# Kernel optimization log

Hardware: AMD Instinct MI355X
Metric: run time of the kernel (lower is better)

## Reference

```python
import jax, jax.numpy as jnp
import numpy as np

N_NODES = 50000
N_EDGES = 800000
D_IN = 64
D_OUT = 64


def setup_inputs() -> dict:
    key = jax.random.key(0)
    ks = jax.random.split(key, 5)
    feat = jax.random.normal(ks[0], (N_NODES, D_IN), dtype=jnp.float32)
    src = jax.random.randint(ks[1], (N_EDGES,), 0, N_NODES, dtype=jnp.int64)
    dst = jax.random.randint(ks[2], (N_EDGES,), 0, N_NODES, dtype=jnp.int64)
    # Xavier-uniform-ish scale for weights
    lim = float(np.sqrt(6.0 / (D_IN + D_OUT)) * np.sqrt(2.0))
    W_neigh = jax.random.uniform(ks[3], (D_OUT, D_IN), dtype=jnp.float32, minval=-lim, maxval=lim)
    W_self = jax.random.uniform(ks[4], (D_OUT, D_IN), dtype=jnp.float32, minval=-lim, maxval=lim)
    b_self = jnp.zeros((D_OUT,), dtype=jnp.float32)
    return {"feat": feat, "src": src, "dst": dst,
            "W_neigh": W_neigh, "W_self": W_self, "b_self": b_self}


def reference(feat, src, dst, W_neigh, W_self, b_self):
    # srcdata = fc_neigh(feat_src)  -> [N, D_OUT]
    srcdata = feat @ W_neigh.T
    # A_div.T @ srcdata == mean of transformed source feats over in-edges per dst.
    # deg[j] = A.sum(0)[j]; column scaling by 1/deg then transpose-SpMM.
    agg = jax.ops.segment_sum(srcdata[src], dst, num_segments=N_NODES)  # [N, D_OUT]
    deg = jax.ops.segment_sum(jnp.ones_like(dst, dtype=srcdata.dtype), dst,
                              num_segments=N_NODES)  # [N]
    # Zero-degree columns stay zero in the sparse product (no stored nonzeros).
    dstdata = jnp.where(deg[:, None] > 0, agg / jnp.maximum(deg, 1.0)[:, None], 0.0)
    # rst = fc_self(feat_dst) + dstdata ; feat_dst = feat[:N_dst] = feat (square A)
    return feat @ W_self.T + b_self + dstdata
```

## Files before the change

### kernel.cpp

```cpp
#include <hip/hip_runtime.h>

#define N_NODES 50000
#define N_EDGES 800000
#define D 64
#define RB 128
#define NBUCK 391
#define CAP 3072
#define PAD 16
#define NFEATBLK 3125
#define GN 64
#define NGBLK 782

typedef __attribute__((ext_vector_type(8))) __bf16 bf16x8;
typedef __attribute__((ext_vector_type(4))) float f32x4;
typedef __attribute__((ext_vector_type(2))) float f32x2;

__device__ inline unsigned f2bf(float f) {
    unsigned b = __builtin_bit_cast(unsigned, f);
    b += 0x7fffu + ((b >> 16) & 1u);
    return b >> 16;
}

__device__ inline void acc16(float* acc, uint4 v) {
    f32x2 a;
    a = __builtin_amdgcn_cvt_pk_f32_fp8((int)v.x, false); acc[0]  += a.x; acc[1]  += a.y;
    a = __builtin_amdgcn_cvt_pk_f32_fp8((int)v.x, true);  acc[2]  += a.x; acc[3]  += a.y;
    a = __builtin_amdgcn_cvt_pk_f32_fp8((int)v.y, false); acc[4]  += a.x; acc[5]  += a.y;
    a = __builtin_amdgcn_cvt_pk_f32_fp8((int)v.y, true);  acc[6]  += a.x; acc[7]  += a.y;
    a = __builtin_amdgcn_cvt_pk_f32_fp8((int)v.z, false); acc[8]  += a.x; acc[9]  += a.y;
    a = __builtin_amdgcn_cvt_pk_f32_fp8((int)v.z, true);  acc[10] += a.x; acc[11] += a.y;
    a = __builtin_amdgcn_cvt_pk_f32_fp8((int)v.w, false); acc[12] += a.x; acc[13] += a.y;
    a = __builtin_amdgcn_cvt_pk_f32_fp8((int)v.w, true);  acc[14] += a.x; acc[15] += a.y;
}

__global__ __launch_bounds__(256) void pre_kernel(const float* __restrict__ feat,
                                                  const float* __restrict__ Wn,
                                                  const float* __restrict__ Ws,
                                                  unsigned short* __restrict__ fb,
                                                  unsigned* __restrict__ fq,
                                                  unsigned short* __restrict__ wnb,
                                                  unsigned short* __restrict__ wsb) {
    int b = blockIdx.x;
    int t = threadIdx.x;
    if (b < NFEATBLK) {
        int i = b * 256 + t;
        float4 v = ((const float4*)feat)[i];
        uint2 o;
        o.x = f2bf(v.x) | (f2bf(v.y) << 16);
        o.y = f2bf(v.z) | (f2bf(v.w) << 16);
        ((uint2*)fb)[i] = o;
        int q = __builtin_amdgcn_cvt_pk_fp8_f32(v.x, v.y, 0, false);
        q = __builtin_amdgcn_cvt_pk_fp8_f32(v.z, v.w, q, true);
        fq[i] = (unsigned)q;
    } else {
        for (int i = t; i < D * D; i += 256) {
            wnb[i] = (unsigned short)f2bf(Wn[i]);
            wsb[i] = (unsigned short)f2bf(Ws[i]);
        }
    }
}

__global__ __launch_bounds__(1024) void passB_kernel(const int* __restrict__ src, const int* __restrict__ dst,
                                                     int* __restrict__ bcursor, unsigned int* __restrict__ ebuf) {
    __shared__ int cnt[NBUCK];
    __shared__ int base[NBUCK];
    int t = threadIdx.x;
    for (int i = t; i < NBUCK; i += 1024) cnt[i] = 0;
    __syncthreads();
    int eb = blockIdx.x * 8192;
    int s_[8], b_[8], dl_[8];
#pragma unroll
    for (int k = 0; k < 8; ++k) {
        int e = eb + k * 1024 + t;
        if (e < N_EDGES) {
            int dv = dst[e];
            s_[k] = src[e];
            b_[k] = dv >> 7;
            dl_[k] = dv & (RB - 1);
            atomicAdd(&cnt[b_[k]], 1);
        } else b_[k] = -1;
    }
    __syncthreads();
    for (int i = t; i < NBUCK; i += 1024) {
        int c = cnt[i];
        base[i] = c ? atomicAdd(&bcursor[i * PAD], c) : 0;
    }
    __syncthreads();
#pragma unroll
    for (int k = 0; k < 8; ++k) {
        if (b_[k] >= 0) {
            int pos = atomicAdd(&base[b_[k]], 1);
            if (pos < CAP)
                ebuf[(size_t)b_[k] * CAP + pos] = (unsigned)s_[k] | ((unsigned)dl_[k] << 16);
        }
    }
}

__global__ __launch_bounds__(256) void sort_kernel(const int* __restrict__ bcursor,
                                                   const unsigned int* __restrict__ ebuf,
                                                   unsigned short* __restrict__ es2,
                                                   int* __restrict__ offs, int* __restrict__ degA) {
    __shared__ int cnt[RB];
    __shared__ int sc[RB];
    __shared__ int cur[RB];
    int t = threadIdx.x;
    int bk = blockIdx.x;
    if (t < RB) cnt[t] = 0;
    __syncthreads();
    int s0 = bk * CAP;
    int n = bcursor[bk * PAD];
    if (n > CAP) n = CAP;
    for (int i = t; i < n; i += 256) atomicAdd(&cnt[ebuf[s0 + i] >> 16], 1);
    __syncthreads();
    int c = (t < RB) ? cnt[t] : 0;
    if (t < RB) sc[t] = c;
    __syncthreads();
    for (int d = 1; d < RB; d <<= 1) {
        int v = (t < RB && t >= d) ? sc[t - d] : 0;
        __syncthreads();
        if (t < RB) sc[t] += v;
        __syncthreads();
    }
    if (t < RB) {
        int ex = sc[t] - c;
        cur[t] = ex;
        int node = bk * RB + t;
        if (node < N_NODES) { offs[node] = s0 + ex; degA[node] = c; }
    }
    __syncthreads();
    for (int i = t; i < n; i += 256) {
        unsigned r = ebuf[s0 + i];
        int p = atomicAdd(&cur[r >> 16], 1);
        es2[s0 + p] = (unsigned short)(r & 0xFFFFu);
    }
}

#define ALD 68
__global__ __launch_bounds__(256) void gather_mfma_kernel(
        const unsigned short* __restrict__ fb, const unsigned char* __restrict__ fq,
        const int* __restrict__ offs, const int* __restrict__ degA,
        const unsigned short* __restrict__ es2,
        const unsigned short* __restrict__ wsb, const unsigned short* __restrict__ wnb,
        const float* __restrict__ bias, float* __restrict__ out) {
    __shared__ float agg[GN * ALD];
    int t = threadIdx.x;
    int ns = t >> 2, p = t & 3;
    int r0 = blockIdx.x * GN;
    int r = r0 + ns;
    int dg = 0, start = 0;
    if (r < N_NODES) { dg = degA[r]; start = offs[r]; }
    float acc[16];
#pragma unroll
    for (int j = 0; j < 16; ++j) acc[j] = 0.f;
    const unsigned char* fqp = fq + p * 16;
    int i = 0;
    for (; i + 4 <= dg; i += 4) {
        unsigned id0 = es2[start + i + 0];
        unsigned id1 = es2[start + i + 1];
        unsigned id2 = es2[start + i + 2];
        unsigned id3 = es2[start + i + 3];
        uint4 v0 = *(const uint4*)(fqp + (size_t)id0 * D);
        uint4 v1 = *(const uint4*)(fqp + (size_t)id1 * D);
        uint4 v2 = *(const uint4*)(fqp + (size_t)id2 * D);
        uint4 v3 = *(const uint4*)(fqp + (size_t)id3 * D);
        acc16(acc, v0); acc16(acc, v1); acc16(acc, v2); acc16(acc, v3);
    }
    for (; i < dg; ++i) {
        unsigned id = es2[start + i];
        uint4 v = *(const uint4*)(fqp + (size_t)id * D);
        acc16(acc, v);
    }
    float inv = (dg > 0) ? 1.0f / (float)dg : 0.f;
#pragma unroll
    for (int j = 0; j < 16; j += 4) {
        float4 o = make_float4(acc[j] * inv, acc[j + 1] * inv, acc[j + 2] * inv, acc[j + 3] * inv);
        *(float4*)(&agg[ns * ALD + p * 16 + j]) = o;
    }
    __syncthreads();
    int w = t >> 6, lane = t & 63;
    int m = lane & 15, quad = lane >> 4;
    int row = r0 + 16 * w + m;
    int rowA = row < N_NODES ? row : N_NODES - 1;
    bf16x8 aS0 = *(const bf16x8*)(fb + (size_t)rowA * D + 0  + quad * 8);
    bf16x8 aS1 = *(const bf16x8*)(fb + (size_t)rowA * D + 32 + quad * 8);
    bf16x8 aA0, aA1;
#pragma unroll
    for (int j = 0; j < 8; ++j) {
        aA0[j] = (__bf16)agg[(16 * w + m) * ALD + 0  + quad * 8 + j];
        aA1[j] = (__bf16)agg[(16 * w + m) * ALD + 32 + quad * 8 + j];
    }
#pragma unroll
    for (int tt = 0; tt < 4; ++tt) {
        int n = 16 * tt + m;
        bf16x8 bS0 = *(const bf16x8*)(wsb + (size_t)n * D + 0  + quad * 8);
        bf16x8 bS1 = *(const bf16x8*)(wsb + (size_t)n * D + 32 + quad * 8);
        bf16x8 bN0 = *(const bf16x8*)(wnb + (size_t)n * D + 0  + quad * 8);
        bf16x8 bN1 = *(const bf16x8*)(wnb + (size_t)n * D + 32 + quad * 8);
        f32x4 c = {0.f, 0.f, 0.f, 0.f};
        c = __builtin_amdgcn_mfma_f32_16x16x32_bf16(aS0, bS0, c, 0, 0, 0);
        c = __builtin_amdgcn_mfma_f32_16x16x32_bf16(aS1, bS1, c, 0, 0, 0);
        c = __builtin_amdgcn_mfma_f32_16x16x32_bf16(aA0, bN0, c, 0, 0, 0);
        c = __builtin_amdgcn_mfma_f32_16x16x32_bf16(aA1, bN1, c, 0, 0, 0);
        float bv = bias[16 * tt + m];
#pragma unroll
        for (int reg = 0; reg < 4; ++reg) {
            int orow = r0 + 16 * w + quad * 4 + reg;
            if (orow < N_NODES)
                out[(size_t)orow * D + 16 * tt + m] = c[reg] + bv;
        }
    }
}

extern "C" void kernel_launch(void* const* d_in, const int* in_sizes, int n_in,
                              void* d_out, int out_size, void* d_ws, size_t ws_size,
                              hipStream_t stream) {
    const float* feat  = (const float*)d_in[0];
    const int*   src   = (const int*)d_in[1];
    const int*   dst   = (const int*)d_in[2];
    const float* Wn    = (const float*)d_in[3];
    const float* Wself = (const float*)d_in[4];
    const float* bself = (const float*)d_in[5];
    float* out = (float*)d_out;

    unsigned short* featb = (unsigned short*)d_ws;
    unsigned*       featq = (unsigned*)(featb + (size_t)N_NODES * D);
    unsigned short* wnb   = (unsigned short*)(featq + (size_t)N_NODES * D / 4);
    unsigned short* wsb   = wnb + D * D;
    unsigned int*   ebuf  = (unsigned int*)(wsb + D * D);
    unsigned short* es2   = (unsigned short*)(ebuf + (size_t)NBUCK * CAP);
    int* bcursor = (int*)(es2 + (size_t)NBUCK * CAP);
    int* offs    = bcursor + NBUCK * PAD;
    int* degA    = offs + N_NODES;

    hipMemsetAsync(bcursor, 0, (size_t)NBUCK * PAD * sizeof(int), stream);

    pre_kernel<<<NFEATBLK + 1, 256, 0, stream>>>(feat, Wn, Wself, featb, featq, wnb, wsb);
    passB_kernel<<<(N_EDGES + 8191) / 8192, 1024, 0, stream>>>(src, dst, bcursor, ebuf);
    sort_kernel<<<NBUCK, 256, 0, stream>>>(bcursor, ebuf, es2, offs, degA);
    gather_mfma_kernel<<<NGBLK, 256, 0, stream>>>(
        featb, (const unsigned char*)featq, offs, degA, es2, wsb, wnb, bself, out);
}
```

Measured before the change: 121.9 us.

## Fuse per-bucket counting sort into gather-MFMA kernel using shared memory

Result: faster. 114.3 us (-6.3%).

```diff
diff --git a/kernel.cpp b/kernel.cpp
--- a/kernel.cpp
+++ b/kernel.cpp
@@ -9,7 +9,6 @@
 #define PAD 16
 #define NFEATBLK 3125
 #define GN 64
-#define NGBLK 782
 
 typedef __attribute__((ext_vector_type(8))) __bf16 bf16x8;
 typedef __attribute__((ext_vector_type(4))) float f32x4;
@@ -96,69 +95,57 @@
     }
 }
 
-__global__ __launch_bounds__(256) void sort_kernel(const int* __restrict__ bcursor,
-                                                   const unsigned int* __restrict__ ebuf,
-                                                   unsigned short* __restrict__ es2,
-                                                   int* __restrict__ offs, int* __restrict__ degA) {
+#define ALD 68
+__global__ __launch_bounds__(256) void gather_mfma_kernel(
+        const unsigned short* __restrict__ fb, const unsigned char* __restrict__ fq,
+        const int* __restrict__ bcursor, const unsigned int* __restrict__ ebuf,
+        const unsigned short* __restrict__ wsb, const unsigned short* __restrict__ wnb,
+        const float* __restrict__ bias, float* __restrict__ out) {
     __shared__ int cnt[RB];
-    __shared__ int sc[RB];
     __shared__ int cur[RB];
+    __shared__ int sorted[CAP];
+    __shared__ float agg[GN * ALD];
     int t = threadIdx.x;
-    int bk = blockIdx.x;
-    if (t < RB) cnt[t] = 0;
-    __syncthreads();
+    int bk = blockIdx.x >> 1;
+    int half = blockIdx.x & 1;
     int s0 = bk * CAP;
     int n = bcursor[bk * PAD];
     if (n > CAP) n = CAP;
+    if (t < RB) cnt[t] = 0;
+    __syncthreads();
     for (int i = t; i < n; i += 256) atomicAdd(&cnt[ebuf[s0 + i] >> 16], 1);
     __syncthreads();
     int c = (t < RB) ? cnt[t] : 0;
-    if (t < RB) sc[t] = c;
+    if (t < RB) cur[t] = c;
     __syncthreads();
     for (int d = 1; d < RB; d <<= 1) {
-        int v = (t < RB && t >= d) ? sc[t - d] : 0;
+        int v = (t < RB && t >= d) ? cur[t - d] : 0;
         __syncthreads();
-        if (t < RB) sc[t] += v;
+        if (t < RB) cur[t] += v;
         __syncthreads();
     }
-    if (t < RB) {
-        int ex = sc[t] - c;
-        cur[t] = ex;
-        int node = bk * RB + t;
-        if (node < N_NODES) { offs[node] = s0 + ex; degA[node] = c; }
-    }
+    if (t < RB) cur[t] -= c;
     __syncthreads();
     for (int i = t; i < n; i += 256) {
         unsigned r = ebuf[s0 + i];
         int p = atomicAdd(&cur[r >> 16], 1);
-        es2[s0 + p] = (unsigned short)(r & 0xFFFFu);
-    }
-}
-
-#define ALD 68
-__global__ __launch_bounds__(256) void gather_mfma_kernel(
-        const unsigned short* __restrict__ fb, const unsigned char* __restrict__ fq,
-        const int* __restrict__ offs, const int* __restrict__ degA,
-        const unsigned short* __restrict__ es2,
-        const unsigned short* __restrict__ wsb, const unsigned short* __restrict__ wnb,
-        const float* __restrict__ bias, float* __restrict__ out) {
-    __shared__ float agg[GN * ALD];
-    int t = threadIdx.x;
+        sorted[p] = (int)(r & 0xFFFFu);
+    }
+    __syncthreads();
     int ns = t >> 2, p = t & 3;
-    int r0 = blockIdx.x * GN;
-    int r = r0 + ns;
-    int dg = 0, start = 0;
-    if (r < N_NODES) { dg = degA[r]; start = offs[r]; }
+    int dl = half * GN + ns;
+    int dg = cnt[dl];
+    int start = cur[dl] - dg;
     float acc[16];
 #pragma unroll
     for (int j = 0; j < 16; ++j) acc[j] = 0.f;
     const unsigned char* fqp = fq + p * 16;
     int i = 0;
     for (; i + 4 <= dg; i += 4) {
-        unsigned id0 = es2[start + i + 0];
-        unsigned id1 = es2[start + i + 1];
-        unsigned id2 = es2[start + i + 2];
-        unsigned id3 = es2[start + i + 3];
+        int id0 = sorted[start + i + 0];
+        int id1 = sorted[start + i + 1];
+        int id2 = sorted[start + i + 2];
+        int id3 = sorted[start + i + 3];
         uint4 v0 = *(const uint4*)(fqp + (size_t)id0 * D);
         uint4 v1 = *(const uint4*)(fqp + (size_t)id1 * D);
         uint4 v2 = *(const uint4*)(fqp + (size_t)id2 * D);
@@ -166,7 +153,7 @@
         acc16(acc, v0); acc16(acc, v1); acc16(acc, v2); acc16(acc, v3);
     }
     for (; i < dg; ++i) {
-        unsigned id = es2[start + i];
+        int id = sorted[start + i];
         uint4 v = *(const uint4*)(fqp + (size_t)id * D);
         acc16(acc, v);
     }
@@ -177,6 +164,7 @@
         *(float4*)(&agg[ns * ALD + p * 16 + j]) = o;
     }
     __syncthreads();
+    int r0 = blockIdx.x * GN;
     int w = t >> 6, lane = t & 63;
     int m = lane & 15, quad = lane >> 4;
     int row = r0 + 16 * w + m;
@@ -191,22 +179,22 @@
     }
 #pragma unroll
     for (int tt = 0; tt < 4; ++tt) {
-        int n = 16 * tt + m;
-        bf16x8 bS0 = *(const bf16x8*)(wsb + (size_t)n * D + 0  + quad * 8);
-        bf16x8 bS1 = *(const bf16x8*)(wsb + (size_t)n * D + 32 + quad * 8);
-        bf16x8 bN0 = *(const bf16x8*)(wnb + (size_t)n * D + 0  + quad * 8);
-        bf16x8 bN1 = *(const bf16x8*)(wnb + (size_t)n * D + 32 + quad * 8);
-        f32x4 c = {0.f, 0.f, 0.f, 0.f};
-        c = __builtin_amdgcn_mfma_f32_16x16x32_bf16(aS0, bS0, c, 0, 0, 0);
-        c = __builtin_amdgcn_mfma_f32_16x16x32_bf16(aS1, bS1, c, 0, 0, 0);
-        c = __builtin_amdgcn_mfma_f32_16x16x32_bf16(aA0, bN0, c, 0, 0, 0);
-        c = __builtin_amdgcn_mfma_f32_16x16x32_bf16(aA1, bN1, c, 0, 0, 0);
+        int nn = 16 * tt + m;
+        bf16x8 bS0 = *(const bf16x8*)(wsb + (size_t)nn * D + 0  + quad * 8);
+        bf16x8 bS1 = *(const bf16x8*)(wsb + (size_t)nn * D + 32 + quad * 8);
+        bf16x8 bN0 = *(const bf16x8*)(wnb + (size_t)nn * D + 0  + quad * 8);
+        bf16x8 bN1 = *(const bf16x8*)(wnb + (size_t)nn * D + 32 + quad * 8);
+        f32x4 cc = {0.f, 0.f, 0.f, 0.f};
+        cc = __builtin_amdgcn_mfma_f32_16x16x32_bf16(aS0, bS0, cc, 0, 0, 0);
+        cc = __builtin_amdgcn_mfma_f32_16x16x32_bf16(aS1, bS1, cc, 0, 0, 0);
+        cc = __builtin_amdgcn_mfma_f32_16x16x32_bf16(aA0, bN0, cc, 0, 0, 0);
+        cc = __builtin_amdgcn_mfma_f32_16x16x32_bf16(aA1, bN1, cc, 0, 0, 0);
         float bv = bias[16 * tt + m];
 #pragma unroll
         for (int reg = 0; reg < 4; ++reg) {
             int orow = r0 + 16 * w + quad * 4 + reg;
             if (orow < N_NODES)
-                out[(size_t)orow * D + 16 * tt + m] = c[reg] + bv;
+                out[(size_t)orow * D + 16 * tt + m] = cc[reg] + bv;
         }
     }
 }
@@ -227,16 +215,12 @@
     unsigned short* wnb   = (unsigned short*)(featq + (size_t)N_NODES * D / 4);
     unsigned short* wsb   = wnb + D * D;
     unsigned int*   ebuf  = (unsigned int*)(wsb + D * D);
-    unsigned short* es2   = (unsigned short*)(ebuf + (size_t)NBUCK * CAP);
-    int* bcursor = (int*)(es2 + (size_t)NBUCK * CAP);
-    int* offs    = bcursor + NBUCK * PAD;
-    int* degA    = offs + N_NODES;
+    int* bcursor = (int*)(ebuf + (size_t)NBUCK * CAP);
 
     hipMemsetAsync(bcursor, 0, (size_t)NBUCK * PAD * sizeof(int), stream);
 
     pre_kernel<<<NFEATBLK + 1, 256, 0, stream>>>(feat, Wn, Wself, featb, featq, wnb, wsb);
     passB_kernel<<<(N_EDGES + 8191) / 8192, 1024, 0, stream>>>(src, dst, bcursor, ebuf);
-    sort_kernel<<<NBUCK, 256, 0, stream>>>(bcursor, ebuf, es2, offs, degA);
-    gather_mfma_kernel<<<NGBLK, 256, 0, stream>>>(
-        featb, (const unsigned char*)featq, offs, degA, es2, wsb, wnb, bself, out);
-}
+    gather_mfma_kernel<<<2 * NBUCK, 256, 0, stream>>>(
+        featb, (const unsigned char*)featq, bcursor, ebuf, wsb, wnb, bself, out);
+}
```
